# Kernel optimization log

Measured on AMD Instinct MI355X. Metric: run time of the kernel, lower is better.

## Reference

```python
import jax, jax.numpy as jnp
import numpy as np

B, C, IMG, NP = 16, 3, 224, 14
PS = IMG // NP              # 16
D = 768                     # hidden_d (= C*PS*PS = input_d)
NH, L, OUT = 12, 12, 1000
DH = D // NH                # 64
MLP = 4 * D
S = NP * NP + 1             # 197 tokens (cls + patches)
EPS = 1e-5


def positional_embeddings(seq_len, dim):
    i = jnp.arange(seq_len, dtype=jnp.float32)[:, None]
    j = jnp.arange(dim, dtype=jnp.float32)[None, :]
    even = jnp.sin(i / 10000 ** (j / dim))
    odd = jnp.cos(i / 10000 ** ((j - 1) / dim))
    return jnp.where(jnp.arange(dim)[None, :] % 2 == 0, even, odd)


def patchify(images):
    # faithful to torch loop: patch = image[:, i*ps:(i+1)*ps, j*ps:(j+1)*ps].flatten()
    n = images.shape[0]
    x = images.reshape(n, C, NP, PS, NP, PS)
    x = x.transpose(0, 2, 4, 1, 3, 5)          # [n, NP, NP, C, PS, PS]
    return x.reshape(n, NP * NP, C * PS * PS)  # channel-major flatten per patch


def layernorm(x, g, b):
    m = jnp.mean(x, -1, keepdims=True)
    v = jnp.mean((x - m) ** 2, -1, keepdims=True)
    return (x - m) * jax.lax.rsqrt(v + EPS) * g + b


def setup_inputs() -> dict:
    key = jax.random.key(0)
    ks = iter(jax.random.split(key, 32))
    r = lambda shape, s=0.02: jax.random.normal(next(ks), shape, jnp.float32) * s
    inp = {
        "images": jax.random.normal(next(ks), (B, C, IMG, IMG), jnp.float32),
        "Wm": r((D, C * PS * PS)), "bm": r((D,)),
        "cls_tok": jax.random.uniform(next(ks), (1, D), jnp.float32),
        "pe": positional_embeddings(S, D),
        "g1": jnp.ones((L, D)), "beta1": jnp.zeros((L, D)),
        "Wq": r((L, NH, DH, D)), "bq": r((L, NH, DH)),
        "Wk": r((L, NH, DH, D)), "bk": r((L, NH, DH)),
        "Wv": r((L, NH, DH, D)), "bv": r((L, NH, DH)),
        "g2": jnp.ones((L, D)), "beta2": jnp.zeros((L, D)),
        "W1": r((L, MLP, D)), "b1": r((L, MLP)),
        "W2": r((L, D, MLP)), "b2": r((L, D)),
        "Wc": r((OUT, D)), "bc": r((OUT,)),
    }
    return inp


def vit_forward(images, Wm, bm, cls_tok, pe, g1, beta1, Wq, bq, Wk, bk, Wv, bv,
                g2, beta2, W1, b1, W2, b2, Wc, bc):
    n = images.shape[0]
    patches = patchify(images)                                    # [n, NP^2, input_d]
    tokens = patches @ Wm.T + bm                                  # [n, NP^2, D]
    cls = jnp.broadcast_to(cls_tok[None], (n, 1, D))
    out = jnp.concatenate([cls, tokens], axis=1) + pe             # [n, S, D]
    scale = 1.0 / jnp.sqrt(jnp.float32(DH))
    for l in range(L):
        x = layernorm(out, g1[l], beta1[l])
        # per-head Linear on FULL token (use_linear_mapping=True)
        q = jnp.einsum('bsd,hed->bhse', x, Wq[l]) + bq[l][None, :, None, :]
        k = jnp.einsum('bsd,hed->bhse', x, Wk[l]) + bk[l][None, :, None, :]
        v = jnp.einsum('bsd,hed->bhse', x, Wv[l]) + bv[l][None, :, None, :]
        att = jax.nn.softmax(jnp.einsum('bhse,bhte->bhst', q, k) * scale, axis=-1)
        o = jnp.einsum('bhst,bhte->bhse', att, v)                 # [n, H, S, DH]
        o = o.transpose(0, 2, 1, 3).reshape(n, S, D)              # hstack heads
        out = out + o
        y = layernorm(out, g2[l], beta2[l])
        h = jax.nn.gelu(y @ W1[l].T + b1[l], approximate=False)
        out = out + h @ W2[l].T + b2[l]
    pooled = out[:, 0]                                            # cls token
    return jax.nn.softmax(pooled @ Wc.T + bc, axis=-1)


def reference(images, Wm, bm, cls_tok, pe, g1, beta1, Wq, bq, Wk, bk, Wv, bv,
              g2, beta2, W1, b1, W2, b2, Wc, bc):
    return vit_forward(images, Wm, bm, cls_tok, pe, g1, beta1, Wq, bq, Wk, bk,
                       Wv, bv, g2, beta2, W1, b1, W2, b2, Wc, bc)
```

## Files before the change

kernel.cpp:

```cpp
#include <hip/hip_runtime.h>
#include <hip/hip_bf16.h>
#include <math.h>

typedef __hip_bfloat16 bf16;
typedef unsigned short ushort_t;
typedef short bf16x8 __attribute__((ext_vector_type(8)));
typedef float f32x4 __attribute__((ext_vector_type(4)));

static constexpr int BATCH = 16;
static constexpr int SEQ   = 197;
static constexpr int NHEAD = 12;
static constexpr int NMLP  = 3072;
static constexpr int NLAYER= 12;
static constexpr int NCLS  = 1000;
static constexpr int NPATCHES = 196;
static constexpr int MPAD  = 3200;

__device__ __forceinline__ ushort_t f2bu(float x) {
    bf16 v = __float2bfloat16(x);
    return *(ushort_t*)&v;
}

__device__ __forceinline__ void load_lds16(const void* g, void* l) {
    __builtin_amdgcn_global_load_lds(
        (const __attribute__((address_space(1))) void*)g,
        (__attribute__((address_space(3))) void*)l, 16, 0, 0);
}

template<int BK, bool SWZ>
__global__ __launch_bounds__(256) void mfma_gemm(
    const ushort_t* __restrict__ A, const ushort_t* __restrict__ B,
    const float* __restrict__ bias, float* __restrict__ Cf,
    bf16* __restrict__ Cb, int M, int N, int K, int mode)
{
    __shared__ ushort_t As[2][128 * BK];
    __shared__ ushort_t Bs[2][128 * BK];

    const int t = threadIdx.x;

    int m0, n0;
    if constexpr (SWZ) {
        const int nbx  = gridDim.x;
        const int nwg  = nbx * gridDim.y;
        const int orig = blockIdx.y * nbx + blockIdx.x;
        const int xcd  = orig & 7;
        const int loc  = orig >> 3;
        const int qq   = nwg >> 3, rr = nwg & 7;
        const int wg   = (xcd < rr ? xcd * (qq + 1) : rr * (qq + 1) + (xcd - rr) * qq) + loc;
        m0 = (wg / nbx) * 128;
        n0 = (wg % nbx) * 128;
    } else {
        m0 = blockIdx.y * 128;
        n0 = blockIdx.x * 128;
    }

    const int wave = t >> 6;
    const int lane = t & 63;
    const int wm   = (wave >> 1) * 64;
    const int wn   = (wave & 1) * 64;
    const int quad = lane >> 4;
    const int l16  = lane & 15;

    f32x4 acc[4][4] = {};
    const int t8 = t * 8;

    if constexpr (BK == 32) {
        const int srow = t >> 2;
        const int sp   = (t & 3) ^ ((srow >> 1) & 3);
        const int skp  = sp * 8;

        const ushort_t* gA0 = A + (size_t)(m0 + srow) * K + skp;
        const ushort_t* gA1 = A + (size_t)(m0 + 64 + srow) * K + ((t & 3) ^ (((srow + 64) >> 1) & 3)) * 8;
        const ushort_t* gB0 = B + (size_t)(n0 + srow) * K + skp;
        const ushort_t* gB1 = B + (size_t)(n0 + 64 + srow) * K + ((t & 3) ^ (((srow + 64) >> 1) & 3)) * 8;

        load_lds16(gA0, &As[0][t8]);
        load_lds16(gA1, &As[0][t8 + 2048]);
        load_lds16(gB0, &Bs[0][t8]);
        load_lds16(gB1, &Bs[0][t8 + 2048]);
        __syncthreads();

        int cur = 0;
        for (int k0 = 0; k0 < K; k0 += 32) {
            if (k0 + 32 < K) {
                const int nb = cur ^ 1;
                const int kn = k0 + 32;
                load_lds16(gA0 + kn, &As[nb][t8]);
                load_lds16(gA1 + kn, &As[nb][t8 + 2048]);
                load_lds16(gB0 + kn, &Bs[nb][t8]);
                load_lds16(gB1 + kn, &Bs[nb][t8 + 2048]);
            }
            bf16x8 af[4], bfr[4];
            #pragma unroll
            for (int i = 0; i < 4; ++i) {
                int row = wm + i * 16 + l16;
                int s = quad ^ ((row >> 1) & 3);
                af[i] = *(const bf16x8*)&As[cur][row * 32 + s * 8];
            }
            #pragma unroll
            for (int j = 0; j < 4; ++j) {
                int row = wn + j * 16 + l16;
                int s = quad ^ ((row >> 1) & 3);
                bfr[j] = *(const bf16x8*)&Bs[cur][row * 32 + s * 8];
            }
            #pragma unroll
            for (int i = 0; i < 4; ++i)
                #pragma unroll
                for (int j = 0; j < 4; ++j)
                    acc[i][j] = __builtin_amdgcn_mfma_f32_16x16x32_bf16(
                        af[i], bfr[j], acc[i][j], 0, 0, 0);
            __syncthreads();
            cur ^= 1;
        }
    } else {
        const int srow = t >> 3;
        const int sw   = ((t & 7) ^ (srow & 7)) * 8;

        const ushort_t* gA[4];
        const ushort_t* gB[4];
        #pragma unroll
        for (int p = 0; p < 4; ++p) {
            gA[p] = A + (size_t)(m0 + p * 32 + srow) * K + sw;
            gB[p] = B + (size_t)(n0 + p * 32 + srow) * K + sw;
        }

        #pragma unroll
        for (int p = 0; p < 4; ++p) {
            load_lds16(gA[p], &As[0][p * 2048 + t8]);
            load_lds16(gB[p], &Bs[0][p * 2048 + t8]);
        }
        __syncthreads();

        int cur = 0;
        for (int k0 = 0; k0 < K; k0 += 64) {
            if (k0 + 64 < K) {
                const int nb = cur ^ 1;
                const int kn = k0 + 64;
                #pragma unroll
                for (int p = 0; p < 4; ++p) {
                    load_lds16(gA[p] + kn, &As[nb][p * 2048 + t8]);
                    load_lds16(gB[p] + kn, &Bs[nb][p * 2048 + t8]);
                }
            }
            #pragma unroll
            for (int kk = 0; kk < 2; ++kk) {
                bf16x8 af[4], bfr[4];
                const int g = kk * 4 + quad;
                #pragma unroll
                for (int i = 0; i < 4; ++i) {
                    int row = wm + i * 16 + l16;
                    af[i] = *(const bf16x8*)&As[cur][row * 64 + (g ^ (row & 7)) * 8];
                }
                #pragma unroll
                for (int j = 0; j < 4; ++j) {
                    int row = wn + j * 16 + l16;
                    bfr[j] = *(const bf16x8*)&Bs[cur][row * 64 + (g ^ (row & 7)) * 8];
                }
                #pragma unroll
                for (int i = 0; i < 4; ++i)
                    #pragma unroll
                    for (int j = 0; j < 4; ++j)
                        acc[i][j] = __builtin_amdgcn_mfma_f32_16x16x32_bf16(
                            af[i], bfr[j], acc[i][j], 0, 0, 0);
            }
            __syncthreads();
            cur ^= 1;
        }
    }

    #pragma unroll
    for (int i = 0; i < 4; ++i) {
        int mrow = m0 + wm + i * 16 + quad * 4;
        #pragma unroll
        for (int j = 0; j < 4; ++j) {
            int col = n0 + wn + j * 16 + l16;
            float bv = bias ? bias[col] : 0.0f;
            #pragma unroll
            for (int r = 0; r < 4; ++r) {
                int m = mrow + r;
                if (m >= M) continue;
                float v = acc[i][j][r] + bv;
                size_t idx = (size_t)m * N + col;
                if (mode == 1) {
                    v = 0.5f * v * (1.0f + erff(v * 0.70710678118654752f));
                    Cb[idx] = __float2bfloat16(v);
                } else if (mode == 2) {
                    Cf[idx] += v;
                } else {
                    Cf[idx] = v;
                }
            }
        }
    }
}

__global__ void f2b_kernel(const float* __restrict__ src, bf16* __restrict__ dst, int n)
{
    int i4 = (blockIdx.x * 256 + threadIdx.x) * 4;
    for (; i4 < n; i4 += gridDim.x * 1024) {
        float4 v = *(const float4*)(src + i4);
        dst[i4 + 0] = __float2bfloat16(v.x);
        dst[i4 + 1] = __float2bfloat16(v.y);
        dst[i4 + 2] = __float2bfloat16(v.z);
        dst[i4 + 3] = __float2bfloat16(v.w);
    }
}

static constexpr int QKV_ELEMS = 3 * 768 * 768;
static constexpr int W1_ELEMS  = 3072 * 768;
static constexpr int CONV_VECS = (QKV_ELEMS + 2 * W1_ELEMS) / 4;
static constexpr int BIAS_VECS = 2304 / 4;

__global__ void convert_layer_kernel(
    const float* __restrict__ Wq, const float* __restrict__ Wk,
    const float* __restrict__ Wv, const float* __restrict__ W1,
    const float* __restrict__ W2, const float* __restrict__ bq,
    const float* __restrict__ bk, const float* __restrict__ bv,
    bf16* __restrict__ wqkv, bf16* __restrict__ w1b, bf16* __restrict__ w2b,
    float* __restrict__ bqkv)
{
    int idx = blockIdx.x * 256 + threadIdx.x;
    if (idx < BIAS_VECS) {
        int j = idx * 4;
        #pragma unroll
        for (int i = 0; i < 4; ++i) {
            int jj = j + i;
            float v = (jj < 768) ? bq[jj] : (jj < 1536) ? bk[jj - 768] : bv[jj - 1536];
            bqkv[jj] = v;
        }
    }
    int w = idx - BIAS_VECS;
    if (w < 0 || w >= CONV_VECS) return;
    const float* src;
    bf16* dst;
    int e;
    if (w < QKV_ELEMS / 4) {
        e = w * 4;
        int tsel = e / (768 * 768);
        int off = e - tsel * 768 * 768;
        src = (tsel == 0 ? Wq : tsel == 1 ? Wk : Wv) + off;
        dst = wqkv + tsel * 768 * 768 + off;
    } else if (w < QKV_ELEMS / 4 + W1_ELEMS / 4) {
        e = (w - QKV_ELEMS / 4) * 4;
        src = W1 + e;
        dst = w1b + e;
    } else {
        e = (w - QKV_ELEMS / 4 - W1_ELEMS / 4) * 4;
        src = W2 + e;
        dst = w2b + e;
    }
    float4 v = *(const float4*)src;
    dst[0] = __float2bfloat16(v.x);
    dst[1] = __float2bfloat16(v.y);
    dst[2] = __float2bfloat16(v.z);
    dst[3] = __float2bfloat16(v.w);
}

__global__ void patchify_kernel(const float* __restrict__ images,
                                bf16* __restrict__ patches, int total)
{
    int idx = blockIdx.x * 256 + threadIdx.x;
    if (idx >= total) return;
    int kidx = idx % 768;
    int p = (idx / 768) % NPATCHES;
    int b = idx / (768 * NPATCHES);
    int c  = kidx >> 8;
    int rem = kidx & 255;
    int iy = rem >> 4, ix = rem & 15;
    int py = p / 14, px = p % 14;
    size_t src = (((size_t)(b * 3 + c) * 224) + py * 16 + iy) * 224 + px * 16 + ix;
    patches[idx] = __float2bfloat16(images[src]);
}

__global__ void assemble_kernel(const float* __restrict__ tokens,
                                const float* __restrict__ cls,
                                const float* __restrict__ pe,
                                float* __restrict__ out, int total)
{
    int idx = blockIdx.x * 256 + threadIdx.x;
    if (idx >= total) return;
    int d = idx % 768;
    int s = (idx / 768) % SEQ;
    int b = idx / (768 * SEQ);
    float v = (s == 0) ? cls[d]
                       : tokens[((size_t)b * NPATCHES + (s - 1)) * 768 + d];
    out[idx] = v + pe[(size_t)s * 768 + d];
}

__global__ __launch_bounds__(256) void ln_kernel(const float* __restrict__ inp,
                                                 const float* __restrict__ g,
                                                 const float* __restrict__ beta,
                                                 bf16* __restrict__ xout)
{
    int r = blockIdx.x;
    const float* rowp = inp + (size_t)r * 768;
    float vals[3];
    float s = 0.f, s2 = 0.f;
    #pragma unroll
    for (int i = 0; i < 3; ++i) {
        float v = rowp[threadIdx.x + 256 * i];
        vals[i] = v; s += v; s2 += v * v;
    }
    __shared__ float rs[256], rs2[256];
    rs[threadIdx.x] = s; rs2[threadIdx.x] = s2;
    __syncthreads();
    for (int st = 128; st; st >>= 1) {
        if (threadIdx.x < st) {
            rs[threadIdx.x]  += rs[threadIdx.x + st];
            rs2[threadIdx.x] += rs2[threadIdx.x + st];
        }
        __syncthreads();
    }
    float mean = rs[0] * (1.0f / 768.0f);
    float var  = rs2[0] * (1.0f / 768.0f) - mean * mean;
    float rstd = rsqrtf(var + 1e-5f);
    #pragma unroll
    for (int i = 0; i < 3; ++i) {
        int d = threadIdx.x + 256 * i;
        xout[(size_t)r * 768 + d] =
            __float2bfloat16((vals[i] - mean) * rstd * g[d] + beta[d]);
    }
}

static constexpr int ATTN_LDS = (224 * 72 + 64 * 232 + 4 * 16 * 232) * 2;

__global__ __launch_bounds__(256) void attn_mfma_kernel(
    const float* __restrict__ qkv, float* __restrict__ out)
{
    extern __shared__ ushort_t smem[];
    ushort_t* Ks = smem;
    ushort_t* Vt = smem + 224 * 72;
    ushort_t* Ps = Vt + 64 * 232;

    const int bh = blockIdx.x;
    const int b = bh / NHEAD, h = bh % NHEAD;
    const int t = threadIdx.x;
    const int wave = t >> 6, lane = t & 63;
    const int quad = lane >> 4, l16 = lane & 15;

    for (int i = t; i < 224 * 16; i += 256) {
        int tr = i >> 4, e4 = (i & 15) << 2;
        float4 kv = {0.f, 0.f, 0.f, 0.f}, vv = {0.f, 0.f, 0.f, 0.f};
        if (tr < SEQ) {
            const float* base = qkv + (size_t)(b * SEQ + tr) * 2304 + h * 64 + e4;
            kv = *(const float4*)(base + 768);
            vv = *(const float4*)(base + 1536);
        }
        ushort_t kp[4] = {f2bu(kv.x), f2bu(kv.y), f2bu(kv.z), f2bu(kv.w)};
        *(uint2*)&Ks[tr * 72 + e4] = *(const uint2*)kp;
        Vt[(e4 + 0) * 232 + tr] = f2bu(vv.x);
        Vt[(e4 + 1) * 232 + tr] = f2bu(vv.y);
        Vt[(e4 + 2) * 232 + tr] = f2bu(vv.z);
        Vt[(e4 + 3) * 232 + tr] = f2bu(vv.w);
    }
    __syncthreads();

    bf16* pw = (bf16*)(Ps + wave * 16 * 232);

    for (int qt = wave; qt < 13; qt += 4) {
        const int q0 = qt * 16;

        bf16x8 qf[2];
        #pragma unroll
        for (int c = 0; c < 2; ++c) {
            const float* qp = qkv + (size_t)(b * SEQ + q0 + l16) * 2304
                            + h * 64 + c * 32 + quad * 8;
            float4 a = *(const float4*)qp;
            float4 b2 = *(const float4*)(qp + 4);
            qf[c][0] = (short)f2bu(a.x);  qf[c][1] = (short)f2bu(a.y);
            qf[c][2] = (short)f2bu(a.z);  qf[c][3] = (short)f2bu(a.w);
            qf[c][4] = (short)f2bu(b2.x); qf[c][5] = (short)f2bu(b2.y);
            qf[c][6] = (short)f2bu(b2.z); qf[c][7] = (short)f2bu(b2.w);
        }

        f32x4 sc[14] = {};
        #pragma unroll
        for (int tt = 0; tt < 14; ++tt) {
            #pragma unroll
            for (int c = 0; c < 2; ++c) {
                bf16x8 kf = *(const bf16x8*)&Ks[(tt * 16 + l16) * 72 + c * 32 + quad * 8];
                sc[tt] = __builtin_amdgcn_mfma_f32_16x16x32_bf16(qf[c], kf, sc[tt], 0, 0, 0);
            }
        }

        f32x4 m4;
        #pragma unroll
        for (int r = 0; r < 4; ++r) m4[r] = -3.4e38f;
        #pragma unroll
        for (int tt = 0; tt < 14; ++tt) {
            int tg = tt * 16 + l16;
            #pragma unroll
            for (int r = 0; r < 4; ++r) {
                sc[tt][r] = (tg < SEQ) ? sc[tt][r] * 0.125f : -1e30f;
                m4[r] = fmaxf(m4[r], sc[tt][r]);
            }
        }
        #pragma unroll
        for (int off = 1; off < 16; off <<= 1)
            #pragma unroll
            for (int r = 0; r < 4; ++r)
                m4[r] = fmaxf(m4[r], __shfl_xor(m4[r], off));

        f32x4 l4 = {};
        #pragma unroll
        for (int tt = 0; tt < 14; ++tt)
            #pragma unroll
            for (int r = 0; r < 4; ++r) {
                float p = __expf(sc[tt][r] - m4[r]);
                sc[tt][r] = p;
                l4[r] += p;
            }
        #pragma unroll
        for (int off = 1; off < 16; off <<= 1)
            #pragma unroll
            for (int r = 0; r < 4; ++r)
                l4[r] += __shfl_xor(l4[r], off);

        #pragma unroll
        for (int tt = 0; tt < 14; ++tt)
            #pragma unroll
            for (int r = 0; r < 4; ++r)
                pw[(quad * 4 + r) * 232 + tt * 16 + l16] = __float2bfloat16(sc[tt][r]);

        f32x4 oa[4] = {};
        #pragma unroll
        for (int c = 0; c < 7; ++c) {
            bf16x8 pf = *(const bf16x8*)&((ushort_t*)pw)[l16 * 232 + c * 32 + quad * 8];
            #pragma unroll
            for (int nt = 0; nt < 4; ++nt) {
                bf16x8 vf = *(const bf16x8*)&Vt[(nt * 16 + l16) * 232 + c * 32 + quad * 8];
                oa[nt] = __builtin_amdgcn_mfma_f32_16x16x32_bf16(pf, vf, oa[nt], 0, 0, 0);
            }
        }

        #pragma unroll
        for (int r = 0; r < 4; ++r) {
            int q = q0 + quad * 4 + r;
            if (q >= SEQ) continue;
            float rl = 1.0f / l4[r];
            float* orow = out + (size_t)(b * SEQ + q) * 768 + h * 64;
            #pragma unroll
            for (int nt = 0; nt < 4; ++nt)
                orow[nt * 16 + l16] += oa[nt][r] * rl;
        }
    }
}

__global__ __launch_bounds__(256) void cls_logits_kernel(
    const float* __restrict__ out, const float* __restrict__ Wc,
    const float* __restrict__ bc, float* __restrict__ logits)
{
    int b = blockIdx.y;
    int j = blockIdx.x * 256 + threadIdx.x;
    __shared__ float pooled[768];
    for (int d = threadIdx.x; d < 768; d += 256)
        pooled[d] = out[(size_t)b * SEQ * 768 + d];
    __syncthreads();
    if (j >= NCLS) return;
    const float* wr = Wc + (size_t)j * 768;
    float acc = 0.f;
    for (int d = 0; d < 768; ++d) acc += pooled[d] * wr[d];
    logits[b * NCLS + j] = acc + bc[j];
}

__global__ __launch_bounds__(256) void cls_softmax_kernel(
    const float* __restrict__ logits, float* __restrict__ dout)
{
    int b = blockIdx.x;
    __shared__ float red[256];
    const float* lg = logits + b * NCLS;

    float m = -3.4e38f;
    for (int j = threadIdx.x; j < NCLS; j += 256) m = fmaxf(m, lg[j]);
    red[threadIdx.x] = m; __syncthreads();
    for (int st = 128; st; st >>= 1) {
        if (threadIdx.x < st) red[threadIdx.x] = fmaxf(red[threadIdx.x], red[threadIdx.x + st]);
        __syncthreads();
    }
    m = red[0]; __syncthreads();

    float ssum = 0.f;
    for (int j = threadIdx.x; j < NCLS; j += 256) ssum += __expf(lg[j] - m);
    red[threadIdx.x] = ssum; __syncthreads();
    for (int st = 128; st; st >>= 1) {
        if (threadIdx.x < st) red[threadIdx.x] += red[threadIdx.x + st];
        __syncthreads();
    }
    float inv = 1.0f / red[0];
    __syncthreads();

    for (int j = threadIdx.x; j < NCLS; j += 256)
        dout[(size_t)b * NCLS + j] = __expf(lg[j] - m) * inv;
}

extern "C" void kernel_launch(void* const* d_in, const int* in_sizes, int n_in,
                              void* d_out, int out_size, void* d_ws, size_t ws_size,
                              hipStream_t stream)
{
    const float* images  = (const float*)d_in[0];
    const float* Wm      = (const float*)d_in[1];
    const float* bm      = (const float*)d_in[2];
    const float* cls_tok = (const float*)d_in[3];
    const float* pe      = (const float*)d_in[4];
    const float* g1      = (const float*)d_in[5];
    const float* beta1   = (const float*)d_in[6];
    const float* Wq      = (const float*)d_in[7];
    const float* bq      = (const float*)d_in[8];
    const float* Wk      = (const float*)d_in[9];
    const float* bk      = (const float*)d_in[10];
    const float* Wv      = (const float*)d_in[11];
    const float* bv      = (const float*)d_in[12];
    const float* g2      = (const float*)d_in[13];
    const float* beta2   = (const float*)d_in[14];
    const float* W1      = (const float*)d_in[15];
    const float* b1      = (const float*)d_in[16];
    const float* W2      = (const float*)d_in[17];
    const float* b2      = (const float*)d_in[18];
    const float* Wc      = (const float*)d_in[19];
    const float* bc      = (const float*)d_in[20];
    float* outp = (float*)d_out;

    const int M  = BATCH * SEQ;
    const int MP = BATCH * NPATCHES;

    char* ws = (char*)d_ws;
    float* out  = (float*)ws; ws += (size_t)MPAD * 768 * 4;
    bf16*  xb   = (bf16*) ws; ws += (size_t)MPAD * 768 * 2;
    float* qkv  = (float*)ws; ws += (size_t)MPAD * 2304 * 4;
    bf16*  h    = (bf16*) ws; ws += (size_t)MPAD * 3072 * 2;
    bf16*  wqkv = (bf16*) ws; ws += (size_t)2304 * 768 * 2;
    bf16*  w1b  = (bf16*) ws; ws += (size_t)3072 * 768 * 2;
    bf16*  w2b  = (bf16*) ws; ws += (size_t)768 * 3072 * 2;
    float* bqkv = (float*)ws; ws += 2304 * 4;
    bf16*  wmb  = (bf16*) ws; ws += (size_t)768 * 768 * 2;
    float* logits = (float*)ws; ws += (size_t)BATCH * NCLS * 4;
    bf16*  patches = (bf16*)h;
    float* tokens  = (float*)((char*)h + (size_t)MPAD * 768 * 2);

    hipFuncSetAttribute((const void*)attn_mfma_kernel,
                        hipFuncAttributeMaxDynamicSharedMemorySize, ATTN_LDS);

    f2b_kernel<<<576, 256, 0, stream>>>(Wm, wmb, 768 * 768);
    int tot_p = MP * 768;
    patchify_kernel<<<(tot_p + 255) / 256, 256, 0, stream>>>(images, patches, tot_p);
    mfma_gemm<64, true><<<dim3(768 / 128, (MP + 127) / 128), 256, 0, stream>>>(
        (const ushort_t*)patches, (const ushort_t*)wmb, bm, tokens, nullptr,
        MP, 768, 768, 0);
    int tot_a = M * 768;
    assemble_kernel<<<(tot_a + 255) / 256, 256, 0, stream>>>(tokens, cls_tok, pe, out, tot_a);

    const int MB = (M + 127) / 128;
    const int conv_blocks = (CONV_VECS + BIAS_VECS + 255) / 256;

    for (int l = 0; l < NLAYER; ++l) {
        convert_layer_kernel<<<conv_blocks, 256, 0, stream>>>(
            Wq + (size_t)l * 768 * 768, Wk + (size_t)l * 768 * 768,
            Wv + (size_t)l * 768 * 768, W1 + (size_t)l * NMLP * 768,
            W2 + (size_t)l * 768 * NMLP, bq + l * 768, bk + l * 768, bv + l * 768,
            wqkv, w1b, w2b, bqkv);

        ln_kernel<<<M, 256, 0, stream>>>(out, g1 + l * 768, beta1 + l * 768, xb);
        mfma_gemm<32, false><<<dim3(2304 / 128, MB), 256, 0, stream>>>(
            (const ushort_t*)xb, (const ushort_t*)wqkv, bqkv, qkv, nullptr,
            M, 2304, 768, 0);
        attn_mfma_kernel<<<BATCH * NHEAD, 256, ATTN_LDS, stream>>>(qkv, out);
        ln_kernel<<<M, 256, 0, stream>>>(out, g2 + l * 768, beta2 + l * 768, xb);
        mfma_gemm<32, false><<<dim3(NMLP / 128, MB), 256, 0, stream>>>(
            (const ushort_t*)xb, (const ushort_t*)w1b, b1 + l * NMLP, nullptr, h,
            M, NMLP, 768, 1);
        mfma_gemm<64, true><<<dim3(768 / 128, MB), 256, 0, stream>>>(
            (const ushort_t*)h, (const ushort_t*)w2b, b2 + l * 768, out, nullptr,
            M, 768, NMLP, 2);
    }

    cls_logits_kernel<<<dim3(4, BATCH), 256, 0, stream>>>(out, Wc, bc, logits);
    cls_softmax_kernel<<<BATCH, 256, 0, stream>>>(logits, outp);
}
```

Baseline: 2.634 ms.

## Add split-K with separate reduction for narrow-N GEMMs

Splits the K dimension four ways for the patch-embedding GEMM and the per-layer W2 down-projection, both of which have N=768 and so launch few workgroups (about 6x25). Each split writes fp32 partial sums to a workspace buffer, and a new reduce kernel sums the four slices, adds the bias and, for W2, accumulates into the residual. This raises the number of workgroups to fill the GPU's compute units. In exchange it adds extra global memory traffic for the partials, one more kernel launch per GEMM, and a larger workspace requirement; it falls back to the old path if the workspace is too small.

```diff
diff --git a/kernel.cpp b/kernel.cpp
--- a/kernel.cpp
+++ b/kernel.cpp
@@ -54,6 +54,9 @@
         n0 = blockIdx.x * 128;
     }
 
+    const int ksp = K / (int)gridDim.z;
+    const int kb  = blockIdx.z * ksp;
+
     const int wave = t >> 6;
     const int lane = t & 63;
     const int wm   = (wave >> 1) * 64;
@@ -69,10 +72,10 @@
         const int sp   = (t & 3) ^ ((srow >> 1) & 3);
         const int skp  = sp * 8;
 
-        const ushort_t* gA0 = A + (size_t)(m0 + srow) * K + skp;
-        const ushort_t* gA1 = A + (size_t)(m0 + 64 + srow) * K + ((t & 3) ^ (((srow + 64) >> 1) & 3)) * 8;
-        const ushort_t* gB0 = B + (size_t)(n0 + srow) * K + skp;
-        const ushort_t* gB1 = B + (size_t)(n0 + 64 + srow) * K + ((t & 3) ^ (((srow + 64) >> 1) & 3)) * 8;
+        const ushort_t* gA0 = A + (size_t)(m0 + srow) * K + skp + kb;
+        const ushort_t* gA1 = A + (size_t)(m0 + 64 + srow) * K + ((t & 3) ^ (((srow + 64) >> 1) & 3)) * 8 + kb;
+        const ushort_t* gB0 = B + (size_t)(n0 + srow) * K + skp + kb;
+        const ushort_t* gB1 = B + (size_t)(n0 + 64 + srow) * K + ((t & 3) ^ (((srow + 64) >> 1) & 3)) * 8 + kb;
 
         load_lds16(gA0, &As[0][t8]);
         load_lds16(gA1, &As[0][t8 + 2048]);
@@ -81,8 +84,8 @@
         __syncthreads();
 
         int cur = 0;
-        for (int k0 = 0; k0 < K; k0 += 32) {
-            if (k0 + 32 < K) {
+        for (int k0 = 0; k0 < ksp; k0 += 32) {
+            if (k0 + 32 < ksp) {
                 const int nb = cur ^ 1;
                 const int kn = k0 + 32;
                 load_lds16(gA0 + kn, &As[nb][t8]);
@@ -120,8 +123,8 @@
         const ushort_t* gB[4];
         #pragma unroll
         for (int p = 0; p < 4; ++p) {
-            gA[p] = A + (size_t)(m0 + p * 32 + srow) * K + sw;
-            gB[p] = B + (size_t)(n0 + p * 32 + srow) * K + sw;
+            gA[p] = A + (size_t)(m0 + p * 32 + srow) * K + sw + kb;
+            gB[p] = B + (size_t)(n0 + p * 32 + srow) * K + sw + kb;
         }
 
         #pragma unroll
@@ -132,8 +135,8 @@
         __syncthreads();
 
         int cur = 0;
-        for (int k0 = 0; k0 < K; k0 += 64) {
-            if (k0 + 64 < K) {
+        for (int k0 = 0; k0 < ksp; k0 += 64) {
+            if (k0 + 64 < ksp) {
                 const int nb = cur ^ 1;
                 const int kn = k0 + 64;
                 #pragma unroll
@@ -168,6 +171,25 @@
         }
     }
 
+    if (gridDim.z > 1) {
+        float* dst = Cf + (size_t)blockIdx.z * M * N;
+        #pragma unroll
+        for (int i = 0; i < 4; ++i) {
+            int mrow = m0 + wm + i * 16 + quad * 4;
+            #pragma unroll
+            for (int j = 0; j < 4; ++j) {
+                int col = n0 + wn + j * 16 + l16;
+                #pragma unroll
+                for (int r = 0; r < 4; ++r) {
+                    int m = mrow + r;
+                    if (m >= M) continue;
+                    dst[(size_t)m * N + col] = acc[i][j][r];
+                }
+            }
+        }
+        return;
+    }
+
     #pragma unroll
     for (int i = 0; i < 4; ++i) {
         int mrow = m0 + wm + i * 16 + quad * 4;
@@ -191,6 +213,30 @@
                 }
             }
         }
+    }
+}
+
+__global__ __launch_bounds__(256) void reduce4_kernel(
+    const float* __restrict__ parts, const float* __restrict__ bias,
+    float* __restrict__ dst, int total, int N, int mode, size_t slice)
+{
+    int i = (blockIdx.x * 256 + threadIdx.x) * 4;
+    for (; i < total; i += gridDim.x * 1024) {
+        float4 v0 = *(const float4*)(parts + i);
+        float4 v1 = *(const float4*)(parts + slice + i);
+        float4 v2 = *(const float4*)(parts + 2 * slice + i);
+        float4 v3 = *(const float4*)(parts + 3 * slice + i);
+        float4 bv = *(const float4*)(bias + (i % N));
+        float4 s;
+        s.x = v0.x + v1.x + v2.x + v3.x + bv.x;
+        s.y = v0.y + v1.y + v2.y + v3.y + bv.y;
+        s.z = v0.z + v1.z + v2.z + v3.z + bv.z;
+        s.w = v0.w + v1.w + v2.w + v3.w + bv.w;
+        if (mode == 2) {
+            float4 o = *(const float4*)(dst + i);
+            s.x += o.x; s.y += o.y; s.z += o.z; s.w += o.w;
+        }
+        *(float4*)(dst + i) = s;
     }
 }
 
@@ -534,6 +580,8 @@
     float* bqkv = (float*)ws; ws += 2304 * 4;
     bf16*  wmb  = (bf16*) ws; ws += (size_t)768 * 768 * 2;
     float* logits = (float*)ws; ws += (size_t)BATCH * NCLS * 4;
+    float* part = (float*)ws; ws += (size_t)4 * M * 768 * 4;
+    const bool can_split = ((size_t)(ws - (char*)d_ws) <= ws_size);
     bf16*  patches = (bf16*)h;
     float* tokens  = (float*)((char*)h + (size_t)MPAD * 768 * 2);
 
@@ -543,9 +591,17 @@
     f2b_kernel<<<576, 256, 0, stream>>>(Wm, wmb, 768 * 768);
     int tot_p = MP * 768;
     patchify_kernel<<<(tot_p + 255) / 256, 256, 0, stream>>>(images, patches, tot_p);
-    mfma_gemm<64, true><<<dim3(768 / 128, (MP + 127) / 128), 256, 0, stream>>>(
-        (const ushort_t*)patches, (const ushort_t*)wmb, bm, tokens, nullptr,
-        MP, 768, 768, 0);
+    if (can_split) {
+        mfma_gemm<64, true><<<dim3(768 / 128, (MP + 127) / 128, 4), 256, 0, stream>>>(
+            (const ushort_t*)patches, (const ushort_t*)wmb, nullptr, part, nullptr,
+            MP, 768, 768, 0);
+        reduce4_kernel<<<1180, 256, 0, stream>>>(part, bm, tokens,
+                                                 MP * 768, 768, 0, (size_t)MP * 768);
+    } else {
+        mfma_gemm<64, true><<<dim3(768 / 128, (MP + 127) / 128), 256, 0, stream>>>(
+            (const ushort_t*)patches, (const ushort_t*)wmb, bm, tokens, nullptr,
+            MP, 768, 768, 0);
+    }
     int tot_a = M * 768;
     assemble_kernel<<<(tot_a + 255) / 256, 256, 0, stream>>>(tokens, cls_tok, pe, out, tot_a);
 
@@ -568,9 +624,17 @@
         mfma_gemm<32, false><<<dim3(NMLP / 128, MB), 256, 0, stream>>>(
             (const ushort_t*)xb, (const ushort_t*)w1b, b1 + l * NMLP, nullptr, h,
             M, NMLP, 768, 1);
-        mfma_gemm<64, true><<<dim3(768 / 128, MB), 256, 0, stream>>>(
-            (const ushort_t*)h, (const ushort_t*)w2b, b2 + l * 768, out, nullptr,
-            M, 768, NMLP, 2);
+        if (can_split) {
+            mfma_gemm<64, true><<<dim3(768 / 128, MB, 4), 256, 0, stream>>>(
+                (const ushort_t*)h, (const ushort_t*)w2b, nullptr, part, nullptr,
+                M, 768, NMLP, 2);
+            reduce4_kernel<<<1184, 256, 0, stream>>>(part, b2 + l * 768, out,
+                                                     M * 768, 768, 2, (size_t)M * 768);
+        } else {
+            mfma_gemm<64, true><<<dim3(768 / 128, MB), 256, 0, stream>>>(
+                (const ushort_t*)h, (const ushort_t*)w2b, b2 + l * 768, out, nullptr,
+                M, 768, NMLP, 2);
+        }
     }
 
     cls_logits_kernel<<<dim3(4, BATCH), 256, 0, stream>>>(out, Wc, bc, logits);
```

Result: faster. 2.257 ms (-14.3%).
